# Optimization experiments

Measured on AMD Instinct MI355X. Metric: run time of the kernel, lower is better.

The kernel has to match this reference:

```python
import jax, jax.numpy as jnp
import numpy as np

H, W, K = 1024, 2048, 64


def _make_xy_coords(h, w):
    # matches torch buffer: xy_coords[0] = x coords (1..w), xy_coords[1] = y coords (1..h)
    x = jnp.tile(jnp.arange(1, w + 1, dtype=jnp.float32)[None, :], (h, 1))
    y = jnp.tile(jnp.arange(1, h + 1, dtype=jnp.float32)[:, None], (1, w))
    return jnp.stack((x, y), 0)  # (2, H, W)


def setup_inputs() -> dict:
    key = jax.random.key(0)
    k1, k2 = jax.random.split(key)
    instance_regressions = jax.random.normal(k1, (2, H, W), dtype=jnp.float32) * 32.0
    # center_coords[:, 0] = y in [0, H), center_coords[:, 1] = x in [0, W)
    u = jax.random.uniform(k2, (K, 2), dtype=jnp.float32)
    center_coords = u * jnp.array([H, W], dtype=jnp.float32)
    xy_coords = _make_xy_coords(H, W)
    return {
        "instance_regressions": instance_regressions,
        "center_coords": center_coords,
        "xy_coords": xy_coords,
    }


def reference(instance_regressions, center_coords, xy_coords):
    # predicted center for every pixel: (2, H, W)
    pred = xy_coords - instance_regressions
    px, py = pred[0], pred[1]                      # (H, W) each
    cy, cx = center_coords[:, 0], center_coords[:, 1]  # (k,) each; note column order
    dx = px[:, :, None] - cx[None, None, :]        # (H, W, k)
    dy = py[:, :, None] - cy[None, None, :]        # (H, W, k)
    dist = jnp.sqrt(dx * dx + dy * dy)             # (H, W, k)
    closest_inds = jnp.argmin(dist, axis=-1) + 1   # (H, W) int, 1-based instance ids
    return closest_inds
```

## Files before the change

### kernel.cpp

```cpp
#include <hip/hip_runtime.h>


#define H_ 1024
#define W_ 2048
#define K_ 64
#define RELW 9.5367431640625e-7f
#define ABSW 4.0f

typedef int ix4 __attribute__((ext_vector_type(4)));

__global__ __launch_bounds__(256) void inst_map_kernel(
    const float* __restrict__ reg,
    const float* __restrict__ cc,
    int* __restrict__ out)
{
    __shared__ float4 cand[4][K_ + 1];

    const int tid  = threadIdx.x;
    const int w    = tid >> 6;
    const int lane = tid & 63;
    const int tr0  = blockIdx.y * 32;
    const int tc0  = blockIdx.x * 32;
    const int r    = tr0 + w * 8 + (lane >> 3);
    const int c    = tc0 + ((lane & 7) << 2);
    const int base = r * W_ + c;

    const float4 rx = *reinterpret_cast<const float4*>(reg + base);
    const float4 ry = *reinterpret_cast<const float4*>(reg + H_ * W_ + base);

    const float ax = (float)tc0 + 16.5f;
    const float ay = (float)(tr0 + w * 8) + 4.5f;

    float pxn[4], pyn[4], h[4];
    {
        const float cshift = (float)c - ax;
        const float rshift = (float)(r + 1) - ay;
        const float rv[4] = {rx.x, rx.y, rx.z, rx.w};
        const float yv[4] = {ry.x, ry.y, ry.z, ry.w};
        #pragma unroll
        for (int i = 0; i < 4; ++i) {
            const float sx = (cshift + (float)(i + 1)) - rv[i];
            const float sy = rshift - yv[i];
            pxn[i] = -2.0f * sx;
            pyn[i] = -2.0f * sy;
            h[i]   = __fmaf_rn(sx, sx, sy * sy);
        }
    }
    float m = fmaxf(fmaxf(h[0], h[1]), fmaxf(h[2], h[3]));

    const float cyk = cc[2 * lane];
    const float cxk = cc[2 * lane + 1];
    const float sxc = cxk - ax, syc = cyk - ay;
    const float ck  = __fmaf_rn(sxc, sxc, syc * syc);
    const float d   = sqrtf(ck);
    float dmin = d;
    #pragma unroll
    for (int s = 1; s < 64; s <<= 1) {
        m    = fmaxf(m,    __shfl_xor(m, s, 64));
        dmin = fminf(dmin, __shfl_xor(dmin, s, 64));
    }

    const bool keep = d <= dmin + 2.0f * sqrtf(m) + 4.0f;
    const unsigned long long mask = __ballot(keep);
    const int ncand = (int)__popcll(mask);
    if (keep) {
        const int pos = (int)__popcll(mask & ((1ull << lane) - 1ull));
        cand[w][pos] = make_float4(sxc, syc, ck, __int_as_float(lane + 1));
    }
    if (lane == 0)
        cand[w][ncand] = make_float4(0.0f, 0.0f, INFINITY, __int_as_float(1));

    float best[4] = {INFINITY, INFINITY, INFINITY, INFINITY};
    float sec[4]  = {INFINITY, INFINITY, INFINITY, INFINITY};
    int   bidx[4] = {1, 1, 1, 1};

    float4 cd = cand[w][0];
    for (int j = 0; j < ncand; ++j) {
        const float4 nx = cand[w][j + 1];
        #pragma unroll
        for (int i = 0; i < 4; ++i) {
            const float g = __fmaf_rn(pxn[i], cd.x,
                            __fmaf_rn(pyn[i], cd.y, cd.z));
            const bool lt = g < best[i];
            const float mn = fminf(sec[i], g);
            sec[i]  = lt ? best[i] : mn;
            best[i] = lt ? g : best[i];
            bidx[i] = lt ? __float_as_int(cd.w) : bidx[i];
        }
        cd = nx;
    }

    bool haz = false;
    #pragma unroll
    for (int i = 0; i < 4; ++i)
        haz = haz | (sec[i] - best[i] <=
                     __fmaf_rn(best[i] + h[i], RELW, ABSW));

    if (__any(haz)) {
        const float4 ex = *reinterpret_cast<const float4*>(reg + base);
        const float4 ey = *reinterpret_cast<const float4*>(reg + H_ * W_ + base);
        const float rv[4] = {ex.x, ex.y, ex.z, ex.w};
        const float yv[4] = {ey.x, ey.y, ey.z, ey.w};
        float px[4], py[4], sb[4];
        int bi2[4];
        const float yf = (float)(r + 1);
        #pragma unroll
        for (int i = 0; i < 4; ++i) {
            px[i] = (float)(c + i + 1) - rv[i];
            py[i] = yf - yv[i];
            sb[i] = INFINITY;
            bi2[i] = 1;
        }
        for (int j = 0; j < ncand; ++j) {
            const int kk = __float_as_int(cand[w][j].w);
            const float ecy = cc[2 * (kk - 1)];
            const float ecx = cc[2 * (kk - 1) + 1];
            #pragma unroll
            for (int i = 0; i < 4; ++i) {
                const float dx = px[i] - ecx;
                const float dy = py[i] - ecy;
                const float s2 = __fsqrt_rn(__fadd_rn(__fmul_rn(dx, dx),
                                                      __fmul_rn(dy, dy)));
                const bool lt = s2 < sb[i];
                sb[i]  = lt ? s2 : sb[i];
                bi2[i] = lt ? kk : bi2[i];
            }
        }
        #pragma unroll
        for (int i = 0; i < 4; ++i) bidx[i] = bi2[i];
    }

    const ix4 o = {bidx[0], bidx[1], bidx[2], bidx[3]};
    __builtin_nontemporal_store(o, reinterpret_cast<ix4*>(out + base));
}

extern "C" void kernel_launch(void* const* d_in, const int* in_sizes, int n_in,
                              void* d_out, int out_size, void* d_ws, size_t ws_size,
                              hipStream_t stream) {
    const float* reg = (const float*)d_in[0];
    const float* cc  = (const float*)d_in[1];
    int* out = (int*)d_out;

    dim3 grid(W_ / 32, H_ / 32);
    inst_map_kernel<<<grid, 256, 0, stream>>>(reg, cc, out);
}
```

Baseline: 83.75 us.

## Replace LDS candidate list with ballot-mask iteration and readlane broadcasts

Drops the shared-memory candidate compaction and instead walks the ballot mask with ctz, broadcasting each candidate's center terms from its owning lane via readlane. This removes the LDS writes and reads and the sentinel entry, and turns the candidate data into scalar values. It also updates the second-best tracking with a single med3 and lowers the absolute tolerance of the hazard check from 4 to 1, so the exact fallback path runs for fewer pixels. The tighter tolerance trades some safety margin in the approximate distance comparison for less fallback work.

```diff
diff --git a/kernel.cpp b/kernel.cpp
--- a/kernel.cpp
+++ b/kernel.cpp
@@ -5,17 +5,19 @@
 #define W_ 2048
 #define K_ 64
 #define RELW 9.5367431640625e-7f
-#define ABSW 4.0f
+#define ABSW 1.0f
 
 typedef int ix4 __attribute__((ext_vector_type(4)));
+
+__device__ __forceinline__ float readlane_f(float v, int lane) {
+    return __int_as_float(__builtin_amdgcn_readlane(__float_as_int(v), lane));
+}
 
 __global__ __launch_bounds__(256) void inst_map_kernel(
     const float* __restrict__ reg,
     const float* __restrict__ cc,
     int* __restrict__ out)
 {
-    __shared__ float4 cand[4][K_ + 1];
-
     const int tid  = threadIdx.x;
     const int w    = tid >> 6;
     const int lane = tid & 63;
@@ -62,39 +64,34 @@
 
     const bool keep = d <= dmin + 2.0f * sqrtf(m) + 4.0f;
     const unsigned long long mask = __ballot(keep);
-    const int ncand = (int)__popcll(mask);
-    if (keep) {
-        const int pos = (int)__popcll(mask & ((1ull << lane) - 1ull));
-        cand[w][pos] = make_float4(sxc, syc, ck, __int_as_float(lane + 1));
-    }
-    if (lane == 0)
-        cand[w][ncand] = make_float4(0.0f, 0.0f, INFINITY, __int_as_float(1));
 
     float best[4] = {INFINITY, INFINITY, INFINITY, INFINITY};
     float sec[4]  = {INFINITY, INFINITY, INFINITY, INFINITY};
     int   bidx[4] = {1, 1, 1, 1};
 
-    float4 cd = cand[w][0];
-    for (int j = 0; j < ncand; ++j) {
-        const float4 nx = cand[w][j + 1];
+    unsigned long long rem = mask;
+    while (rem) {
+        const int lj = (int)__builtin_ctzll(rem);
+        rem &= rem - 1ull;
+        const float cxj = readlane_f(sxc, lj);
+        const float cyj = readlane_f(syc, lj);
+        const float ckj = readlane_f(ck,  lj);
+        const int   kk  = lj + 1;
         #pragma unroll
         for (int i = 0; i < 4; ++i) {
-            const float g = __fmaf_rn(pxn[i], cd.x,
-                            __fmaf_rn(pyn[i], cd.y, cd.z));
+            const float g = __fmaf_rn(pxn[i], cxj,
+                            __fmaf_rn(pyn[i], cyj, ckj));
             const bool lt = g < best[i];
-            const float mn = fminf(sec[i], g);
-            sec[i]  = lt ? best[i] : mn;
-            best[i] = lt ? g : best[i];
-            bidx[i] = lt ? __float_as_int(cd.w) : bidx[i];
+            sec[i]  = __builtin_amdgcn_fmed3f(g, best[i], sec[i]);
+            best[i] = fminf(best[i], g);
+            bidx[i] = lt ? kk : bidx[i];
         }
-        cd = nx;
     }
 
     bool haz = false;
     #pragma unroll
     for (int i = 0; i < 4; ++i)
-        haz = haz | (sec[i] - best[i] <=
-                     __fmaf_rn(best[i] + h[i], RELW, ABSW));
+        haz = haz | (sec[i] - best[i] <= __fmaf_rn(best[i] + h[i], RELW, ABSW));
 
     if (__any(haz)) {
         const float4 ex = *reinterpret_cast<const float4*>(reg + base);
@@ -111,10 +108,12 @@
             sb[i] = INFINITY;
             bi2[i] = 1;
         }
-        for (int j = 0; j < ncand; ++j) {
-            const int kk = __float_as_int(cand[w][j].w);
-            const float ecy = cc[2 * (kk - 1)];
-            const float ecx = cc[2 * (kk - 1) + 1];
+        unsigned long long rem2 = mask;
+        while (rem2) {
+            const int lj = (int)__builtin_ctzll(rem2);
+            rem2 &= rem2 - 1ull;
+            const float ecy = cc[2 * lj];
+            const float ecx = cc[2 * lj + 1];
             #pragma unroll
             for (int i = 0; i < 4; ++i) {
                 const float dx = px[i] - ecx;
@@ -123,7 +122,7 @@
                                                       __fmul_rn(dy, dy)));
                 const bool lt = s2 < sb[i];
                 sb[i]  = lt ? s2 : sb[i];
-                bi2[i] = lt ? kk : bi2[i];
+                bi2[i] = lt ? (lj + 1) : bi2[i];
             }
         }
         #pragma unroll
```

New measurement: 82.99 us. No clear change (-0.9%).
